# Kernel optimization log

Measured on AMD Instinct MI355X. Metric: run time of the kernel, lower is better.

## Reference

```python
import jax, jax.numpy as jnp
import numpy as np
from jax import lax

T = 20            # obs_len + pred_len
S = 256           # number of scenes (segments in seq_start_end)
P = 128           # pedestrians per scene (segments equal-sized for vectorization)
B = S * P         # total pedestrians in batch
MLP = 1024
THR = 0.25        # collision_threshold == minimum_distance
BN_EPS = 1e-5


def setup_inputs() -> dict:
    key = jax.random.key(0)
    k = jax.random.split(key, 8)
    traj = jax.random.uniform(k[0], (T, B, 2), jnp.float32) * 15.0  # positions in meters
    traj_rel = jax.random.normal(k[1], (T, B, 2), jnp.float32)
    starts = jnp.arange(S, dtype=jnp.int32) * P
    seq_start_end = jnp.stack([starts, starts + P], axis=1)  # (S, 2)
    W1 = jax.random.normal(k[2], (1, MLP), jnp.float32)
    b1 = jnp.zeros((MLP,), jnp.float32)
    g1 = jnp.ones((MLP,), jnp.float32)
    beta1 = jnp.zeros((MLP,), jnp.float32)
    W2 = jax.random.normal(k[3], (MLP, 1), jnp.float32) / np.sqrt(MLP)
    b2 = jnp.zeros((1,), jnp.float32)
    g2 = jnp.ones((1,), jnp.float32)
    beta2 = jnp.zeros((1,), jnp.float32)
    return dict(traj=traj, traj_rel=traj_rel, seq_start_end=seq_start_end,
                W1=W1, b1=b1, g1=g1, beta1=beta1, W2=W2, b2=b2, g2=g2, beta2=beta2)


def _batchnorm(x, g, b):
    # nn.BatchNorm1d in train mode: biased batch stats
    mean = jnp.mean(x, axis=0)
    var = jnp.var(x, axis=0)
    return g * (x - mean) * lax.rsqrt(var + BN_EPS) + b


def _collision_rewards(traj):
    # traj: (T, B, 2); segments are equal-sized (P peds per scene) -> reshape
    x = traj.reshape(T, S, P, 2)
    diff = x[:, :, :, None, :] - x[:, :, None, :, :]          # (T,S,P,P,2)
    d = jnp.sqrt(jnp.sum(diff * diff, axis=-1))               # (T,S,P,P) pairwise L2
    d = jnp.where(d == 0.0, THR, d)                           # distance[distance==0]=minimum_distance
    m = jnp.min(jnp.min(d, axis=2), axis=0)                   # min over other peds, then time -> (S,P)
    cols = (m < THR).astype(jnp.float32).reshape(B)           # binary collision indicator
    rewards = (1.0 - cols)[:, None]                           # -1*cols + 1, shape (B,1)
    return lax.stop_gradient(rewards)  # binary threshold: no gradient flows to traj


def reference(traj, traj_rel, seq_start_end, W1, b1, g1, beta1, W2, b2, g2, beta2):
    rewards = _collision_rewards(traj)                        # (B,1)
    h = jax.nn.relu(_batchnorm(rewards @ W1 + b1, g1, beta1)) # Linear->BN->ReLU
    out = jax.nn.relu(_batchnorm(h @ W2 + b2, g2, beta2))     # Linear->BN->ReLU
    return out                                                # (B,1) scores
```

## Files before the change

### kernel.cpp

```cpp
#include <hip/hip_runtime.h>

#define TT 20
#define SS 256
#define PP 128
#define BB (SS * PP)
#define MLPD 1024
#define BN_EPS 1e-5f
#define THR_BITS 0x3D800000u

__global__ __launch_bounds__(512) void collide_kernel(
    const float* __restrict__ traj, unsigned* __restrict__ flags) {
  __shared__ float2 sp[TT * PP];
  __shared__ unsigned red[512];
  const int s = blockIdx.x;
  const int tid = threadIdx.x;

  const float2* g = (const float2*)traj;
  for (int k = tid; k < TT * PP; k += 512) {
    int t = k >> 7;
    int ped = k & 127;
    sp[k] = g[(size_t)t * BB + s * PP + ped];
  }
  __syncthreads();

  const int i = tid & 127;
  const int q = tid >> 7;
  unsigned mn = 0xFFFFFFFFu;
#pragma unroll
  for (int tt = 0; tt < 5; ++tt) {
    const int t = q * 5 + tt;
    const float2 pi = sp[t * PP + i];
    const float xi = pi.x, yi = pi.y;
#pragma unroll 8
    for (int j = 0; j < PP; ++j) {
      float2 pj = sp[t * PP + j];
      float dx = __fsub_rn(xi, pj.x);
      float dy = __fsub_rn(yi, pj.y);
      float d2 = __fadd_rn(__fmul_rn(dx, dx), __fmul_rn(dy, dy));
      unsigned u = __float_as_uint(d2) - 1u;
      mn = (u < mn) ? u : mn;
    }
  }
  red[tid] = mn;
  __syncthreads();
  if (tid < 128) {
    unsigned m0 = red[tid];
    unsigned m1 = red[tid + 128];
    unsigned m2 = red[tid + 256];
    unsigned m3 = red[tid + 384];
    unsigned a = m0 < m1 ? m0 : m1;
    unsigned b = m2 < m3 ? m2 : m3;
    unsigned m = a < b ? a : b;
    flags[s * PP + tid] = (m < (THR_BITS - 1u)) ? 1u : 0u;
  }
}

__global__ __launch_bounds__(1024) void mlp_kernel(
    const unsigned* __restrict__ flags,
    const float* __restrict__ W1, const float* __restrict__ b1,
    const float* __restrict__ g1, const float* __restrict__ beta1,
    const float* __restrict__ W2, const float* __restrict__ b2,
    const float* __restrict__ g2, const float* __restrict__ beta2,
    float* __restrict__ outvals) {
  __shared__ float red0[1024];
  __shared__ float red1[1024];
  __shared__ float sh_p;
  const int tid = threadIdx.x;

  const uint4* f4 = (const uint4*)flags;
  unsigned cnt = 0;
#pragma unroll
  for (int k = 0; k < 8; ++k) {
    uint4 v = f4[tid + k * 1024];
    cnt += v.x + v.y + v.z + v.w;
  }
  red0[tid] = (float)cnt;
  __syncthreads();
  for (int off = 512; off > 0; off >>= 1) {
    if (tid < off) red0[tid] += red0[tid + off];
    __syncthreads();
  }
  if (tid == 0) {
    float ncoll = red0[0];
    sh_p = ((float)BB - ncoll) / (float)BB;
  }
  __syncthreads();
  const float p = sh_p;

  float w = W1[tid], gg = g1[tid], bt = beta1[tid], w2 = W2[tid];
  float rs1 = rsqrtf(p * (1.0f - p) * w * w + BN_EPS);
  float h0 = fmaxf(gg * (-p * w) * rs1 + bt, 0.0f);
  float h1 = fmaxf(gg * ((1.0f - p) * w) * rs1 + bt, 0.0f);
  red0[tid] = h0 * w2;
  red1[tid] = h1 * w2;
  __syncthreads();
  for (int off = 512; off > 0; off >>= 1) {
    if (tid < off) {
      red0[tid] += red0[tid + off];
      red1[tid] += red1[tid + off];
    }
    __syncthreads();
  }
  if (tid == 0) {
    float z0 = red0[0] + b2[0];
    float z1 = red1[0] + b2[0];
    float dz = z1 - z0;
    float rs2 = rsqrtf(p * (1.0f - p) * dz * dz + BN_EPS);
    float o0 = fmaxf(g2[0] * (p * (z0 - z1)) * rs2 + beta2[0], 0.0f);
    float o1 = fmaxf(g2[0] * ((1.0f - p) * dz) * rs2 + beta2[0], 0.0f);
    outvals[0] = o0;
    outvals[1] = o1;
  }
}

__global__ __launch_bounds__(256) void scatter_kernel(
    const unsigned* __restrict__ flags, const float* __restrict__ outvals,
    float* __restrict__ out) {
  int gid = blockIdx.x * 256 + threadIdx.x;
  float o0 = outvals[0];
  float o1 = outvals[1];
  out[gid] = flags[gid] ? o0 : o1;
}

extern "C" void kernel_launch(void* const* d_in, const int* in_sizes, int n_in,
                              void* d_out, int out_size, void* d_ws, size_t ws_size,
                              hipStream_t stream) {
  const float* traj = (const float*)d_in[0];
  const float* W1 = (const float*)d_in[3];
  const float* b1 = (const float*)d_in[4];
  const float* g1 = (const float*)d_in[5];
  const float* beta1 = (const float*)d_in[6];
  const float* W2 = (const float*)d_in[7];
  const float* b2 = (const float*)d_in[8];
  const float* g2 = (const float*)d_in[9];
  const float* beta2 = (const float*)d_in[10];

  unsigned* flags = (unsigned*)d_ws;
  float* outvals = (float*)((char*)d_ws + BB * sizeof(unsigned));
  float* out = (float*)d_out;

  collide_kernel<<<SS, 512, 0, stream>>>(traj, flags);
  mlp_kernel<<<1, 1024, 0, stream>>>(flags, W1, b1, g1, beta1, W2, b2, g2,
                                     beta2, outvals);
  scatter_kernel<<<BB / 256, 256, 0, stream>>>(flags, outvals, out);
}
```

Before: 96.85 us.

## Pack collision flags as per-scene bitmasks in output buffer, precount per scene

The collide kernel now ballots collision flags into per-scene 128-bit masks and a per-scene collision count, and stores them in the output buffer itself instead of a workspace flag array. The MLP kernel reads only 256 per-scene counts rather than the full 32K-entry flag array, and stashes the two output values into each scene's slot. The scatter kernel then expands the bits per scene. This cuts global memory traffic for flags. It relies on the scatter step reading each block's header before overwriting it, which holds because every block touches only its own 128-float slice.

```diff
diff --git a/kernel.cpp b/kernel.cpp
--- a/kernel.cpp
+++ b/kernel.cpp
@@ -9,9 +9,10 @@
 #define THR_BITS 0x3D800000u
 
 __global__ __launch_bounds__(512) void collide_kernel(
-    const float* __restrict__ traj, unsigned* __restrict__ flags) {
+    const float* __restrict__ traj, float* __restrict__ out) {
   __shared__ float2 sp[TT * PP];
   __shared__ unsigned red[512];
+  __shared__ unsigned wcnt[2];
   const int s = blockIdx.x;
   const int tid = threadIdx.x;
 
@@ -51,29 +52,39 @@
     unsigned a = m0 < m1 ? m0 : m1;
     unsigned b = m2 < m3 ? m2 : m3;
     unsigned m = a < b ? a : b;
-    flags[s * PP + tid] = (m < (THR_BITS - 1u)) ? 1u : 0u;
+    int pred = (m < (THR_BITS - 1u)) ? 1 : 0;
+    unsigned long long mask = __ballot(pred);
+    unsigned* ob = (unsigned*)(out + (size_t)s * PP);
+    if (tid == 0) {
+      ob[0] = (unsigned)mask;
+      ob[1] = (unsigned)(mask >> 32);
+      wcnt[0] = (unsigned)__popcll(mask);
+    }
+    if (tid == 64) {
+      ob[2] = (unsigned)mask;
+      ob[3] = (unsigned)(mask >> 32);
+      wcnt[1] = (unsigned)__popcll(mask);
+    }
+  }
+  __syncthreads();
+  if (tid == 0) {
+    ((unsigned*)(out + (size_t)s * PP))[8] = wcnt[0] + wcnt[1];
   }
 }
 
 __global__ __launch_bounds__(1024) void mlp_kernel(
-    const unsigned* __restrict__ flags,
+    float* __restrict__ out,
     const float* __restrict__ W1, const float* __restrict__ b1,
     const float* __restrict__ g1, const float* __restrict__ beta1,
     const float* __restrict__ W2, const float* __restrict__ b2,
-    const float* __restrict__ g2, const float* __restrict__ beta2,
-    float* __restrict__ outvals) {
+    const float* __restrict__ g2, const float* __restrict__ beta2) {
   __shared__ float red0[1024];
   __shared__ float red1[1024];
-  __shared__ float sh_p;
+  __shared__ float sh_p, sh_o0, sh_o1;
   const int tid = threadIdx.x;
 
-  const uint4* f4 = (const uint4*)flags;
   unsigned cnt = 0;
-#pragma unroll
-  for (int k = 0; k < 8; ++k) {
-    uint4 v = f4[tid + k * 1024];
-    cnt += v.x + v.y + v.z + v.w;
-  }
+  if (tid < SS) cnt = ((const unsigned*)out)[(size_t)tid * PP + 8];
   red0[tid] = (float)cnt;
   __syncthreads();
   for (int off = 512; off > 0; off >>= 1) {
@@ -106,20 +117,28 @@
     float z1 = red1[0] + b2[0];
     float dz = z1 - z0;
     float rs2 = rsqrtf(p * (1.0f - p) * dz * dz + BN_EPS);
-    float o0 = fmaxf(g2[0] * (p * (z0 - z1)) * rs2 + beta2[0], 0.0f);
-    float o1 = fmaxf(g2[0] * ((1.0f - p) * dz) * rs2 + beta2[0], 0.0f);
-    outvals[0] = o0;
-    outvals[1] = o1;
+    sh_o0 = fmaxf(g2[0] * (p * (z0 - z1)) * rs2 + beta2[0], 0.0f);
+    sh_o1 = fmaxf(g2[0] * ((1.0f - p) * dz) * rs2 + beta2[0], 0.0f);
+  }
+  __syncthreads();
+  if (tid < SS) {
+    out[(size_t)tid * PP + 126] = sh_o0;
+    out[(size_t)tid * PP + 127] = sh_o1;
   }
 }
 
-__global__ __launch_bounds__(256) void scatter_kernel(
-    const unsigned* __restrict__ flags, const float* __restrict__ outvals,
-    float* __restrict__ out) {
-  int gid = blockIdx.x * 256 + threadIdx.x;
-  float o0 = outvals[0];
-  float o1 = outvals[1];
-  out[gid] = flags[gid] ? o0 : o1;
+__global__ __launch_bounds__(128) void scatter_kernel(float* __restrict__ out) {
+  __shared__ unsigned fw[4];
+  __shared__ float so0, so1;
+  const int s = blockIdx.x;
+  const int tid = threadIdx.x;
+  float* base = out + (size_t)s * PP;
+  if (tid < 4) fw[tid] = ((const unsigned*)base)[tid];
+  if (tid == 4) so0 = base[126];
+  if (tid == 5) so1 = base[127];
+  __syncthreads();
+  unsigned bit = (fw[tid >> 5] >> (tid & 31)) & 1u;
+  base[tid] = bit ? so0 : so1;
 }
 
 extern "C" void kernel_launch(void* const* d_in, const int* in_sizes, int n_in,
@@ -135,12 +154,10 @@
   const float* g2 = (const float*)d_in[9];
   const float* beta2 = (const float*)d_in[10];
 
-  unsigned* flags = (unsigned*)d_ws;
-  float* outvals = (float*)((char*)d_ws + BB * sizeof(unsigned));
+  (void)d_ws; (void)ws_size;
   float* out = (float*)d_out;
 
-  collide_kernel<<<SS, 512, 0, stream>>>(traj, flags);
-  mlp_kernel<<<1, 1024, 0, stream>>>(flags, W1, b1, g1, beta1, W2, b2, g2,
-                                     beta2, outvals);
-  scatter_kernel<<<BB / 256, 256, 0, stream>>>(flags, outvals, out);
+  collide_kernel<<<SS, 512, 0, stream>>>(traj, out);
+  mlp_kernel<<<1, 1024, 0, stream>>>(out, W1, b1, g1, beta1, W2, b2, g2, beta2);
+  scatter_kernel<<<SS, 128, 0, stream>>>(out);
 }
```

New measurement: 96.76 us. No clear change (-0.1%).

## Fuse MLP and scatter, emit per-scene counts and ballot bitmasks from collision kernel

Applied to the files above, without the earlier changes.

The collision kernel now uses 640 threads, each wave covering two timesteps with two pedestrians per lane and sharing each pj load between them. It writes per-scene collision counts and ballot bitmasks in place of a per-pedestrian flag array. The separate single-block MLP kernel and the scatter kernel are merged into one 256-block kernel. Each block reduces the 256 counts, recomputes the tiny MLP redundantly and writes its scene's outputs, which removes one launch and the serial single-block stage at the cost of duplicated MLP work per block.

```diff
diff --git a/kernel.cpp b/kernel.cpp
--- a/kernel.cpp
+++ b/kernel.cpp
@@ -4,85 +4,108 @@
 #define SS 256
 #define PP 128
 #define BB (SS * PP)
-#define MLPD 1024
 #define BN_EPS 1e-5f
 #define THR_BITS 0x3D800000u
 
-__global__ __launch_bounds__(512) void collide_kernel(
-    const float* __restrict__ traj, unsigned* __restrict__ flags) {
+
+__global__ __launch_bounds__(640) void collide_kernel(
+    const float* __restrict__ traj, unsigned* __restrict__ ws) {
   __shared__ float2 sp[TT * PP];
-  __shared__ unsigned red[512];
+  __shared__ unsigned redu[10 * PP];
+  __shared__ unsigned wc[2];
   const int s = blockIdx.x;
   const int tid = threadIdx.x;
 
   const float2* g = (const float2*)traj;
-  for (int k = tid; k < TT * PP; k += 512) {
+  for (int k = tid; k < TT * PP; k += 640) {
     int t = k >> 7;
     int ped = k & 127;
     sp[k] = g[(size_t)t * BB + s * PP + ped];
   }
   __syncthreads();
 
-  const int i = tid & 127;
-  const int q = tid >> 7;
-  unsigned mn = 0xFFFFFFFFu;
+  const int w = tid >> 6;
+  const int l = tid & 63;
+  const int t0 = 2 * w;
+
+  const float2 pa0 = sp[t0 * PP + l];
+  const float2 pb0 = sp[t0 * PP + 64 + l];
+  const float2 pa1 = sp[(t0 + 1) * PP + l];
+  const float2 pb1 = sp[(t0 + 1) * PP + 64 + l];
+
+  unsigned mnA = 0xFFFFFFFFu, mnB = 0xFFFFFFFFu;
+
+#define PAIR_LOOP(XA, YA, XB, YB, TROW)                                  \
+  {                                                                      \
+    const float2* row = &sp[(TROW)*PP];                                  \
+    _Pragma("unroll 8") for (int j = 0; j < PP; ++j) {                   \
+      float2 pj = row[j];     \
+      float dxa = __fsub_rn(XA, pj.x);                                   \
+      float dxb = __fsub_rn(XB, pj.x);                                   \
+      float dya = __fsub_rn(YA, pj.y);                                   \
+      float dyb = __fsub_rn(YB, pj.y);                                   \
+      float sa = __fadd_rn(__fmul_rn(dxa, dxa), __fmul_rn(dya, dya));    \
+      float sb = __fadd_rn(__fmul_rn(dxb, dxb), __fmul_rn(dyb, dyb));    \
+      unsigned ua = __float_as_uint(sa) - 1u;                            \
+      unsigned ub = __float_as_uint(sb) - 1u;                            \
+      mnA = (ua < mnA) ? ua : mnA;                                       \
+      mnB = (ub < mnB) ? ub : mnB;                                       \
+    }                                                                    \
+  }
+
+  PAIR_LOOP(pa0.x, pa0.y, pb0.x, pb0.y, t0)
+  PAIR_LOOP(pa1.x, pa1.y, pb1.x, pb1.y, t0 + 1)
+#undef PAIR_LOOP
+
+  redu[w * PP + l] = mnA;
+  redu[w * PP + 64 + l] = mnB;
+  __syncthreads();
+
+  if (tid < PP) {
+    unsigned m = redu[tid];
 #pragma unroll
-  for (int tt = 0; tt < 5; ++tt) {
-    const int t = q * 5 + tt;
-    const float2 pi = sp[t * PP + i];
-    const float xi = pi.x, yi = pi.y;
-#pragma unroll 8
-    for (int j = 0; j < PP; ++j) {
-      float2 pj = sp[t * PP + j];
-      float dx = __fsub_rn(xi, pj.x);
-      float dy = __fsub_rn(yi, pj.y);
-      float d2 = __fadd_rn(__fmul_rn(dx, dx), __fmul_rn(dy, dy));
-      unsigned u = __float_as_uint(d2) - 1u;
-      mn = (u < mn) ? u : mn;
+    for (int ww = 1; ww < 10; ++ww) {
+      unsigned v = redu[ww * PP + tid];
+      m = (v < m) ? v : m;
+    }
+    int pred = (m < (THR_BITS - 1u)) ? 1 : 0;
+    unsigned long long mask = __ballot(pred);
+    if (l == 0) {
+      int half = tid >> 6;
+      ws[256 + s * 4 + half * 2 + 0] = (unsigned)mask;
+      ws[256 + s * 4 + half * 2 + 1] = (unsigned)(mask >> 32);
+      wc[half] = (unsigned)__popcll(mask);
     }
   }
-  red[tid] = mn;
   __syncthreads();
-  if (tid < 128) {
-    unsigned m0 = red[tid];
-    unsigned m1 = red[tid + 128];
-    unsigned m2 = red[tid + 256];
-    unsigned m3 = red[tid + 384];
-    unsigned a = m0 < m1 ? m0 : m1;
-    unsigned b = m2 < m3 ? m2 : m3;
-    unsigned m = a < b ? a : b;
-    flags[s * PP + tid] = (m < (THR_BITS - 1u)) ? 1u : 0u;
-  }
+  if (tid == 0) ws[s] = wc[0] + wc[1];
 }
 
-__global__ __launch_bounds__(1024) void mlp_kernel(
-    const unsigned* __restrict__ flags,
+__global__ __launch_bounds__(512) void mlp_scatter_kernel(
+    const unsigned* __restrict__ ws,
     const float* __restrict__ W1, const float* __restrict__ b1,
     const float* __restrict__ g1, const float* __restrict__ beta1,
     const float* __restrict__ W2, const float* __restrict__ b2,
     const float* __restrict__ g2, const float* __restrict__ beta2,
-    float* __restrict__ outvals) {
-  __shared__ float red0[1024];
-  __shared__ float red1[1024];
-  __shared__ float sh_p;
+    float* __restrict__ out) {
+  __shared__ float r0[512];
+  __shared__ float r1[512];
+  __shared__ unsigned scnt[8];
+  __shared__ unsigned smask[4];
+  __shared__ float sh_p, sh_o0, sh_o1;
+  const int s = blockIdx.x;
   const int tid = threadIdx.x;
 
-  const uint4* f4 = (const uint4*)flags;
-  unsigned cnt = 0;
+  if (tid < 4) smask[tid] = ws[256 + s * 4 + tid];
+
+  unsigned csum = (tid < SS) ? ws[tid] : 0u;
 #pragma unroll
-  for (int k = 0; k < 8; ++k) {
-    uint4 v = f4[tid + k * 1024];
-    cnt += v.x + v.y + v.z + v.w;
-  }
-  red0[tid] = (float)cnt;
+  for (int off = 32; off; off >>= 1) csum += __shfl_xor(csum, off, 64);
+  if ((tid & 63) == 0) scnt[tid >> 6] = csum;
   __syncthreads();
-  for (int off = 512; off > 0; off >>= 1) {
-    if (tid < off) red0[tid] += red0[tid + off];
-    __syncthreads();
-  }
   if (tid == 0) {
-    float ncoll = red0[0];
-    sh_p = ((float)BB - ncoll) / (float)BB;
+    unsigned total = scnt[0] + scnt[1] + scnt[2] + scnt[3];
+    sh_p = ((float)BB - (float)total) / (float)BB;
   }
   __syncthreads();
   const float p = sh_p;
@@ -91,35 +114,44 @@
   float rs1 = rsqrtf(p * (1.0f - p) * w * w + BN_EPS);
   float h0 = fmaxf(gg * (-p * w) * rs1 + bt, 0.0f);
   float h1 = fmaxf(gg * ((1.0f - p) * w) * rs1 + bt, 0.0f);
-  red0[tid] = h0 * w2;
-  red1[tid] = h1 * w2;
+  float c0 = h0 * w2, c1 = h1 * w2;
+
+  int k2 = tid + 512;
+  float wB = W1[k2], ggB = g1[k2], btB = beta1[k2], w2B = W2[k2];
+  float rs1B = rsqrtf(p * (1.0f - p) * wB * wB + BN_EPS);
+  float h0B = fmaxf(ggB * (-p * wB) * rs1B + btB, 0.0f);
+  float h1B = fmaxf(ggB * ((1.0f - p) * wB) * rs1B + btB, 0.0f);
+
+  r0[tid] = c0 + h0B * w2B;
+  r1[tid] = c1 + h1B * w2B;
   __syncthreads();
-  for (int off = 512; off > 0; off >>= 1) {
-    if (tid < off) {
-      red0[tid] += red0[tid + off];
-      red1[tid] += red1[tid + off];
+  if (tid < 256) { r0[tid] += r0[tid + 256]; r1[tid] += r1[tid + 256]; }
+  __syncthreads();
+  if (tid < 128) { r0[tid] += r0[tid + 128]; r1[tid] += r1[tid + 128]; }
+  __syncthreads();
+  if (tid < 64) {
+    float a0 = r0[tid] + r0[tid + 64];
+    float a1 = r1[tid] + r1[tid + 64];
+#pragma unroll
+    for (int off = 32; off; off >>= 1) {
+      a0 += __shfl_xor(a0, off, 64);
+      a1 += __shfl_xor(a1, off, 64);
     }
-    __syncthreads();
+    if (tid == 0) {
+      float z0 = a0 + b2[0];
+      float z1 = a1 + b2[0];
+      float dz = z1 - z0;
+      float rs2 = rsqrtf(p * (1.0f - p) * dz * dz + BN_EPS);
+      sh_o0 = fmaxf(g2[0] * (p * (z0 - z1)) * rs2 + beta2[0], 0.0f);
+      sh_o1 = fmaxf(g2[0] * ((1.0f - p) * dz) * rs2 + beta2[0], 0.0f);
+    }
   }
-  if (tid == 0) {
-    float z0 = red0[0] + b2[0];
-    float z1 = red1[0] + b2[0];
-    float dz = z1 - z0;
-    float rs2 = rsqrtf(p * (1.0f - p) * dz * dz + BN_EPS);
-    float o0 = fmaxf(g2[0] * (p * (z0 - z1)) * rs2 + beta2[0], 0.0f);
-    float o1 = fmaxf(g2[0] * ((1.0f - p) * dz) * rs2 + beta2[0], 0.0f);
-    outvals[0] = o0;
-    outvals[1] = o1;
+  __syncthreads();
+
+  if (tid < PP) {
+    unsigned bit = (smask[tid >> 5] >> (tid & 31)) & 1u;
+    out[(size_t)s * PP + tid] = bit ? sh_o0 : sh_o1;
   }
-}
-
-__global__ __launch_bounds__(256) void scatter_kernel(
-    const unsigned* __restrict__ flags, const float* __restrict__ outvals,
-    float* __restrict__ out) {
-  int gid = blockIdx.x * 256 + threadIdx.x;
-  float o0 = outvals[0];
-  float o1 = outvals[1];
-  out[gid] = flags[gid] ? o0 : o1;
 }
 
 extern "C" void kernel_launch(void* const* d_in, const int* in_sizes, int n_in,
@@ -135,12 +167,10 @@
   const float* g2 = (const float*)d_in[9];
   const float* beta2 = (const float*)d_in[10];
 
-  unsigned* flags = (unsigned*)d_ws;
-  float* outvals = (float*)((char*)d_ws + BB * sizeof(unsigned));
+  unsigned* ws = (unsigned*)d_ws;
   float* out = (float*)d_out;
 
-  collide_kernel<<<SS, 512, 0, stream>>>(traj, flags);
-  mlp_kernel<<<1, 1024, 0, stream>>>(flags, W1, b1, g1, beta1, W2, b2, g2,
-                                     beta2, outvals);
-  scatter_kernel<<<BB / 256, 256, 0, stream>>>(flags, outvals, out);
+  collide_kernel<<<SS, 640, 0, stream>>>(traj, ws);
+  mlp_scatter_kernel<<<SS, 512, 0, stream>>>(ws, W1, b1, g1, beta1, W2, b2, g2,
+                                             beta2, out);
 }
```

Measured after the change: 92.87 us. 1.04x faster.
